# Kernel optimization log

Measured on AMD Instinct MI355X. Metric: run time of the kernel, lower is better.

## Reference

```python
import jax, jax.numpy as jnp
import numpy as np
from jax import lax

B, C, IMG = 16, 3, 256
NH, NRH, K, D = 128, 32, 512, 64
COMMITMENT = 0.25
DN = ('NCHW', 'OIHW', 'NCHW')


def _conv(x, w, b=None, stride=1, pad=1):
    out = lax.conv_general_dilated(x, w, (stride, stride), [(pad, pad), (pad, pad)], dimension_numbers=DN)
    if b is not None:
        out = out + b[None, :, None, None]
    return out


def _res(x, wa, wb):
    # Residual: x + ReLU(Conv1x1(ReLU(Conv3x3(x)))), convs bias-free
    h = jax.nn.relu(_conv(x, wa, None, 1, 1))
    h = jax.nn.relu(_conv(h, wb, None, 1, 0))
    return x + h


def _convT(x, w, b):
    # PyTorch ConvTranspose2d(k=4, s=2, p=1); w is torch layout (Cin, Cout, 4, 4)
    k = jnp.flip(w, (2, 3)).transpose(1, 0, 2, 3)  # -> OIHW
    out = lax.conv_general_dilated(x, k, (1, 1), [(2, 2), (2, 2)], lhs_dilation=(2, 2), dimension_numbers=DN)
    return out + b[None, :, None, None]


def setup_inputs():
    ks = iter(jax.random.split(jax.random.key(0), 32))
    def rn(shape, s=0.02):
        return jax.random.normal(next(ks), shape, jnp.float32) * s
    return dict(
        x=jax.random.normal(next(ks), (B, C, IMG, IMG), jnp.float32),
        emb=jax.random.uniform(next(ks), (K, D), jnp.float32, -1.0 / K, 1.0 / K),
        ew1=rn((NH // 2, C, 4, 4)), eb1=jnp.zeros((NH // 2,), jnp.float32),
        ew2=rn((NH, NH // 2, 4, 4)), eb2=jnp.zeros((NH,), jnp.float32),
        er1a=rn((NRH, NH, 3, 3)), er1b=rn((NH, NRH, 1, 1)),
        er2a=rn((NRH, NH, 3, 3)), er2b=rn((NH, NRH, 1, 1)),
        ew3=rn((D, NH, 3, 3)), eb3=jnp.zeros((D,), jnp.float32),
        dw1=rn((NH, D, 3, 3)), db1=jnp.zeros((NH,), jnp.float32),
        dr1a=rn((NRH, NH, 3, 3)), dr1b=rn((NH, NRH, 1, 1)),
        dr2a=rn((NRH, NH, 3, 3)), dr2b=rn((NH, NRH, 1, 1)),
        dtw1=rn((NH, NH // 2, 4, 4)), dtb1=jnp.zeros((NH // 2,), jnp.float32),
        dtw2=rn((NH // 2, C, 4, 4)), dtb2=jnp.zeros((C,), jnp.float32),
    )


def reference(x, emb, ew1, eb1, ew2, eb2, er1a, er1b, er2a, er2b, ew3, eb3,
              dw1, db1, dr1a, dr1b, dr2a, dr2b, dtw1, dtb1, dtw2, dtb2):
    # ---- encoder ----
    h = jax.nn.relu(_conv(x, ew1, eb1, 2, 1))
    h = jax.nn.relu(_conv(h, ew2, eb2, 2, 1))
    h = _res(h, er1a, er1b)
    h = _res(h, er2a, er2b)
    z = _conv(h, ew3, eb3, 1, 1)  # [B, D, H', W']

    # ---- vector quantization ----
    inputs = z.transpose(0, 2, 3, 1)              # BHWC
    flat = inputs.reshape(-1, emb.shape[1])        # [N, D]
    dist = (jnp.sum(flat ** 2, axis=1, keepdims=True)
            + jnp.sum(emb ** 2, axis=1)
            - 2.0 * flat @ emb.T)                  # [N, K]
    idx = jnp.argmin(dist, axis=1)                 # [N]
    quantized = emb[idx].reshape(inputs.shape)     # gather == one-hot matmul

    e_latent_loss = jnp.mean((lax.stop_gradient(quantized) - inputs) ** 2)
    q_latent_loss = jnp.mean((quantized - lax.stop_gradient(inputs)) ** 2)
    vq_loss = q_latent_loss + COMMITMENT * e_latent_loss

    quantized = inputs + lax.stop_gradient(quantized - inputs)  # straight-through
    q = quantized.transpose(0, 3, 1, 2)            # back to NCHW

    # ---- decoder ----
    h = _conv(q, dw1, db1, 1, 1)
    h = _res(h, dr1a, dr1b)
    h = _res(h, dr2a, dr2b)
    h = jax.nn.relu(_convT(h, dtw1, dtb1))
    out = jax.nn.relu(_convT(h, dtw2, dtb2))
    return out, vq_loss
```

## Files before the change

### kernel.cpp

```cpp
#include <hip/hip_runtime.h>

static __device__ __forceinline__ float frelu(float v) { return v > 0.f ? v : 0.f; }

__global__ __launch_bounds__(256) void k_ew1(const float* __restrict__ x,
    const float* __restrict__ w, const float* __restrict__ bias, float* __restrict__ out)
{
    const int t = threadIdx.x;
    const int tile = blockIdx.x;
    const int bcg = blockIdx.y;
    const int b = bcg >> 3, cg = bcg & 7;
    const int oy0 = (tile >> 3) << 4, ox0 = (tile & 7) << 4;
    const int tx = t & 15, ty = t >> 4;
    const int iy0 = 2 * oy0 - 1, ix0 = 2 * ox0 - 1;

    __shared__ float s_in[3 * 34 * 35];
    for (int i = t; i < 3 * 1156; i += 256) {
        int ci = i / 1156, r = (i % 1156) / 34, c = i % 34;
        int gy = iy0 + r, gx = ix0 + c;
        float v = 0.f;
        if ((unsigned)gy < 256u && (unsigned)gx < 256u)
            v = x[((b * 3 + ci) * 256 + gy) * 256 + gx];
        s_in[(ci * 34 + r) * 35 + c] = v;
    }
    __syncthreads();

    float acc[8];
#pragma unroll
    for (int i = 0; i < 8; ++i) acc[i] = 0.f;
#pragma unroll
    for (int ci = 0; ci < 3; ++ci)
#pragma unroll
        for (int ky = 0; ky < 4; ++ky)
#pragma unroll
            for (int kx = 0; kx < 4; ++kx) {
                float v = s_in[(ci * 34 + 2 * ty + ky) * 35 + 2 * tx + kx];
#pragma unroll
                for (int co = 0; co < 8; ++co)
                    acc[co] += v * w[((cg * 8 + co) * 3 + ci) * 16 + ky * 4 + kx];
            }
#pragma unroll
    for (int co = 0; co < 8; ++co) {
        int oc = cg * 8 + co;
        out[((b * 64 + oc) * 128 + oy0 + ty) * 128 + ox0 + tx] = frelu(acc[co] + bias[oc]);
    }
}

__global__ __launch_bounds__(256) void k_ew2(const float* __restrict__ in,
    const float* __restrict__ w, const float* __restrict__ bias, float* __restrict__ out)
{
    const int t = threadIdx.x;
    const int tile = blockIdx.x;
    const int bcg = blockIdx.y;
    const int b = bcg >> 4, cg = bcg & 15;
    const int oy0 = (tile >> 2) << 4, ox0 = (tile & 3) << 4;
    const int tx = t & 15, ty = t >> 4;
    const int iy0 = 2 * oy0 - 1, ix0 = 2 * ox0 - 1;

    __shared__ float s_in[4 * 34 * 35];
    float acc[8];
#pragma unroll
    for (int i = 0; i < 8; ++i) acc[i] = 0.f;

    for (int cc = 0; cc < 16; ++cc) {
        __syncthreads();
        for (int i = t; i < 4 * 1156; i += 256) {
            int ci = i / 1156, r = (i % 1156) / 34, c = i % 34;
            int gy = iy0 + r, gx = ix0 + c;
            float v = 0.f;
            if ((unsigned)gy < 128u && (unsigned)gx < 128u)
                v = in[((b * 64 + cc * 4 + ci) * 128 + gy) * 128 + gx];
            s_in[(ci * 34 + r) * 35 + c] = v;
        }
        __syncthreads();
#pragma unroll
        for (int ci = 0; ci < 4; ++ci)
#pragma unroll
            for (int ky = 0; ky < 4; ++ky)
#pragma unroll
                for (int kx = 0; kx < 4; ++kx) {
                    float v = s_in[(ci * 34 + 2 * ty + ky) * 35 + 2 * tx + kx];
#pragma unroll
                    for (int co = 0; co < 8; ++co)
                        acc[co] += v * w[((cg * 8 + co) * 64 + cc * 4 + ci) * 16 + ky * 4 + kx];
                }
    }
#pragma unroll
    for (int co = 0; co < 8; ++co) {
        int oc = cg * 8 + co;
        out[((b * 128 + oc) * 64 + oy0 + ty) * 64 + ox0 + tx] = frelu(acc[co] + bias[oc]);
    }
}

template<int CIN, int COUT, bool RELU, bool HASBIAS>
__global__ __launch_bounds__(256) void k_conv3(const float* __restrict__ in,
    const float* __restrict__ w, const float* __restrict__ bias, float* __restrict__ out)
{
    const int t = threadIdx.x;
    const int tile = blockIdx.x;
    const int bcg = blockIdx.y;
    const int b = bcg / (COUT / 8), cg = bcg % (COUT / 8);
    const int oy0 = (tile >> 2) << 4, ox0 = (tile & 3) << 4;
    const int tx = t & 15, ty = t >> 4;
    const int iy0 = oy0 - 1, ix0 = ox0 - 1;

    __shared__ float s_in[8 * 18 * 19];
    float acc[8];
#pragma unroll
    for (int i = 0; i < 8; ++i) acc[i] = 0.f;

    for (int cc = 0; cc < CIN / 8; ++cc) {
        __syncthreads();
        for (int i = t; i < 8 * 324; i += 256) {
            int ci = i / 324, r = (i % 324) / 18, c = i % 18;
            int gy = iy0 + r, gx = ix0 + c;
            float v = 0.f;
            if ((unsigned)gy < 64u && (unsigned)gx < 64u)
                v = in[((b * CIN + cc * 8 + ci) * 64 + gy) * 64 + gx];
            s_in[(ci * 18 + r) * 19 + c] = v;
        }
        __syncthreads();
#pragma unroll
        for (int ci = 0; ci < 8; ++ci)
#pragma unroll
            for (int ky = 0; ky < 3; ++ky)
#pragma unroll
                for (int kx = 0; kx < 3; ++kx) {
                    float v = s_in[(ci * 18 + ty + ky) * 19 + tx + kx];
#pragma unroll
                    for (int co = 0; co < 8; ++co)
                        acc[co] += v * w[((cg * 8 + co) * CIN + cc * 8 + ci) * 9 + ky * 3 + kx];
                }
    }
#pragma unroll
    for (int co = 0; co < 8; ++co) {
        int oc = cg * 8 + co;
        float v = acc[co];
        if (HASBIAS) v += bias[oc];
        if (RELU) v = frelu(v);
        out[((b * COUT + oc) * 64 + oy0 + ty) * 64 + ox0 + tx] = v;
    }
}

__global__ __launch_bounds__(256) void k_res1x1(const float* __restrict__ tin,
    const float* __restrict__ w, float* __restrict__ xbuf)
{
    int gid = blockIdx.x * 256 + threadIdx.x;
    int px = gid & 4095;
    int cg = (gid >> 12) & 7;
    int b = gid >> 15;
    float acc[16];
#pragma unroll
    for (int i = 0; i < 16; ++i) acc[i] = 0.f;
#pragma unroll
    for (int ci = 0; ci < 32; ++ci) {
        float v = tin[(b * 32 + ci) * 4096 + px];
#pragma unroll
        for (int co = 0; co < 16; ++co)
            acc[co] += v * w[(cg * 16 + co) * 32 + ci];
    }
#pragma unroll
    for (int co = 0; co < 16; ++co) {
        int o = (b * 128 + cg * 16 + co) * 4096 + px;
        xbuf[o] = xbuf[o] + frelu(acc[co]);
    }
}

__global__ __launch_bounds__(256) void k_vq(const float* __restrict__ z,
    const float* __restrict__ emb, int* __restrict__ idx, float* __restrict__ part)
{
    const int t = threadIdx.x;
    const int p = blockIdx.x * 256 + t;
    const int b = p >> 12, h = (p >> 6) & 63, wq = p & 63;
    float zr[64];
#pragma unroll
    for (int d = 0; d < 64; ++d)
        zr[d] = z[((b * 64 + d) * 64 + h) * 64 + wq];

    __shared__ float se[64 * 64];
    float best = 3.4e38f;
    int bi = 0;
    for (int ch = 0; ch < 8; ++ch) {
        __syncthreads();
#pragma unroll
        for (int i = 0; i < 16; ++i)
            se[i * 256 + t] = emb[ch * 4096 + i * 256 + t];
        __syncthreads();
        for (int e = 0; e < 64; ++e) {
            float dist = 0.f;
#pragma unroll
            for (int d = 0; d < 64; ++d) {
                float diff = zr[d] - se[e * 64 + d];
                dist += diff * diff;
            }
            if (dist < best) { best = dist; bi = ch * 64 + e; }
        }
    }
    idx[p] = bi;

    float s = best;
#pragma unroll
    for (int off = 32; off > 0; off >>= 1) s += __shfl_down(s, off, 64);
    __shared__ float sw[4];
    if ((t & 63) == 0) sw[t >> 6] = s;
    __syncthreads();
    if (t == 0) part[blockIdx.x] = sw[0] + sw[1] + sw[2] + sw[3];
}

__global__ __launch_bounds__(256) void k_qbuild(const int* __restrict__ idx,
    const float* __restrict__ emb, float* __restrict__ q)
{
    int i = blockIdx.x * 256 + threadIdx.x;
    int wq = i & 63;
    int h = (i >> 6) & 63;
    int d = (i >> 12) & 63;
    int b = i >> 18;
    int p = (b << 12) | (h << 6) | wq;
    q[i] = emb[idx[p] * 64 + d];
}

__global__ __launch_bounds__(256) void k_loss(const float* __restrict__ part, float* __restrict__ out)
{
    int t = threadIdx.x;
    float s = part[t];
#pragma unroll
    for (int off = 32; off > 0; off >>= 1) s += __shfl_down(s, off, 64);
    __shared__ float sw[4];
    if ((t & 63) == 0) sw[t >> 6] = s;
    __syncthreads();
    if (t == 0) out[3145728] = 1.25f * (sw[0] + sw[1] + sw[2] + sw[3]) / 4194304.0f;
}

template<int CIN, int COUT, int COT, int OW>
__global__ __launch_bounds__(256) void k_convT(const float* __restrict__ in,
    const float* __restrict__ w, const float* __restrict__ bias, float* __restrict__ out)
{
    const int IW = OW / 2;
    const int TPR = OW / 32;
    const int t = threadIdx.x;
    const int tile = blockIdx.x;
    const int NCG = COUT / COT;
    const int bcg = blockIdx.y;
    const int b = bcg / NCG, cg = bcg % NCG;
    const int oy0 = (tile / TPR) * 32, ox0 = (tile % TPR) * 32;
    const int tx = t & 15, ty = t >> 4;
    const int iy0 = oy0 / 2 - 1, ix0 = ox0 / 2 - 1;

    __shared__ float s_in[8 * 18 * 19];
    float acc[4][COT];
#pragma unroll
    for (int a = 0; a < 4; ++a)
#pragma unroll
        for (int c = 0; c < COT; ++c) acc[a][c] = 0.f;

    for (int cc = 0; cc < CIN / 8; ++cc) {
        __syncthreads();
        for (int i = t; i < 8 * 324; i += 256) {
            int ci = i / 324, r = (i % 324) / 18, c = i % 18;
            int gy = iy0 + r, gx = ix0 + c;
            float v = 0.f;
            if ((unsigned)gy < (unsigned)IW && (unsigned)gx < (unsigned)IW)
                v = in[((b * CIN + cc * 8 + ci) * IW + gy) * IW + gx];
            s_in[(ci * 18 + r) * 19 + c] = v;
        }
        __syncthreads();
#pragma unroll
        for (int ci = 0; ci < 8; ++ci) {
            float rr[3][3];
#pragma unroll
            for (int dy = 0; dy < 3; ++dy)
#pragma unroll
                for (int dx = 0; dx < 3; ++dx)
                    rr[dy][dx] = s_in[(ci * 18 + ty + dy) * 19 + tx + dx];
#pragma unroll
            for (int ky = 0; ky < 4; ++ky) {
                const int py = 1 - (ky & 1);
                const int dy = (ky == 0) ? 2 : (ky == 3) ? 0 : 1;
#pragma unroll
                for (int kx = 0; kx < 4; ++kx) {
                    const int pxr = 1 - (kx & 1);
                    const int dx = (kx == 0) ? 2 : (kx == 3) ? 0 : 1;
                    float v = rr[dy][dx];
#pragma unroll
                    for (int co = 0; co < COT; ++co)
                        acc[py * 2 + pxr][co] +=
                            v * w[((cc * 8 + ci) * COUT + cg * COT + co) * 16 + ky * 4 + kx];
                }
            }
        }
    }
    const int ye = oy0 + 2 * ty, xe = ox0 + 2 * tx;
#pragma unroll
    for (int py = 0; py < 2; ++py)
#pragma unroll
        for (int pxr = 0; pxr < 2; ++pxr)
#pragma unroll
            for (int co = 0; co < COT; ++co) {
                int oc = cg * COT + co;
                out[((b * COUT + oc) * OW + ye + py) * OW + xe + pxr] =
                    frelu(acc[py * 2 + pxr][co] + bias[oc]);
            }
}

extern "C" void kernel_launch(void* const* d_in, const int* in_sizes, int n_in,
                              void* d_out, int out_size, void* d_ws, size_t ws_size,
                              hipStream_t stream)
{
    (void)in_sizes; (void)n_in; (void)out_size; (void)ws_size;
    const float* x    = (const float*)d_in[0];
    const float* emb  = (const float*)d_in[1];
    const float* ew1  = (const float*)d_in[2];
    const float* eb1  = (const float*)d_in[3];
    const float* ew2  = (const float*)d_in[4];
    const float* eb2  = (const float*)d_in[5];
    const float* er1a = (const float*)d_in[6];
    const float* er1b = (const float*)d_in[7];
    const float* er2a = (const float*)d_in[8];
    const float* er2b = (const float*)d_in[9];
    const float* ew3w = (const float*)d_in[10];
    const float* eb3  = (const float*)d_in[11];
    const float* dw1  = (const float*)d_in[12];
    const float* db1  = (const float*)d_in[13];
    const float* dr1a = (const float*)d_in[14];
    const float* dr1b = (const float*)d_in[15];
    const float* dr2a = (const float*)d_in[16];
    const float* dr2b = (const float*)d_in[17];
    const float* dtw1 = (const float*)d_in[18];
    const float* dtb1 = (const float*)d_in[19];
    const float* dtw2 = (const float*)d_in[20];
    const float* dtb2 = (const float*)d_in[21];
    float* out = (float*)d_out;
    float* ws  = (float*)d_ws;

    float* A   = ws;
    float* Bf  = ws + 16777216;
    float* T   = ws;
    float* Z   = ws + 2097152;
    float* Q   = ws + 6291456;
    int*   IDX = (int*)(ws + 10485760);
    float* PART= ws + 10551296;

    k_ew1<<<dim3(64, 128), 256, 0, stream>>>(x, ew1, eb1, A);
    k_ew2<<<dim3(16, 256), 256, 0, stream>>>(A, ew2, eb2, Bf);
    k_conv3<128, 32, true, false><<<dim3(16, 64), 256, 0, stream>>>(Bf, er1a, nullptr, T);
    k_res1x1<<<2048, 256, 0, stream>>>(T, er1b, Bf);
    k_conv3<128, 32, true, false><<<dim3(16, 64), 256, 0, stream>>>(Bf, er2a, nullptr, T);
    k_res1x1<<<2048, 256, 0, stream>>>(T, er2b, Bf);
    k_conv3<128, 64, false, true><<<dim3(16, 128), 256, 0, stream>>>(Bf, ew3w, eb3, Z);
    k_vq<<<256, 256, 0, stream>>>(Z, emb, IDX, PART);
    k_qbuild<<<16384, 256, 0, stream>>>(IDX, emb, Q);
    k_loss<<<1, 256, 0, stream>>>(PART, out);
    k_conv3<64, 128, false, true><<<dim3(16, 256), 256, 0, stream>>>(Q, dw1, db1, Bf);
    k_conv3<128, 32, true, false><<<dim3(16, 64), 256, 0, stream>>>(Bf, dr1a, nullptr, T);
    k_res1x1<<<2048, 256, 0, stream>>>(T, dr1b, Bf);
    k_conv3<128, 32, true, false><<<dim3(16, 64), 256, 0, stream>>>(Bf, dr2a, nullptr, T);
    k_res1x1<<<2048, 256, 0, stream>>>(T, dr2b, Bf);
    k_convT<128, 64, 8, 128><<<dim3(16, 128), 256, 0, stream>>>(Bf, dtw1, dtb1, A);
    k_convT<64, 3, 3, 256><<<dim3(64, 16), 256, 0, stream>>>(A, dtw2, dtb2, out);
}
```

Measured before the change: 2.810 ms.

## Widen output-channel tiles, prefetch inputs into registers, split VQ search and tile q-build

Several kernels now compute more output channels per thread: ew1 does all 64, ew2 and several conv3 and convT launches do 16. This cuts redundant input tile loads and block count. Each conv kernel now prefetches the next channel chunk into registers while computing the current one, and ew2 stores its input tile in a parity-split (polyphase) layout. The VQ search is split across four codebook slices plus a reduce kernel to raise parallelism, and q-build transposes through shared memory for coalesced writes. The trade-off is more registers per thread, which can lower occupancy.

Measured after the change: 8.076 ms. 2.87x slower.

```diff
diff --git a/kernel.cpp b/kernel.cpp
--- a/kernel.cpp
+++ b/kernel.cpp
@@ -7,15 +7,14 @@
 {
     const int t = threadIdx.x;
     const int tile = blockIdx.x;
-    const int bcg = blockIdx.y;
-    const int b = bcg >> 3, cg = bcg & 7;
+    const int b = blockIdx.y;
     const int oy0 = (tile >> 3) << 4, ox0 = (tile & 7) << 4;
     const int tx = t & 15, ty = t >> 4;
     const int iy0 = 2 * oy0 - 1, ix0 = 2 * ox0 - 1;
 
     __shared__ float s_in[3 * 34 * 35];
     for (int i = t; i < 3 * 1156; i += 256) {
-        int ci = i / 1156, r = (i % 1156) / 34, c = i % 34;
+        int ci = i / 1156, rem = i % 1156, r = rem / 34, c = rem % 34;
         int gy = iy0 + r, gx = ix0 + c;
         float v = 0.f;
         if ((unsigned)gy < 256u && (unsigned)gx < 256u)
@@ -24,25 +23,26 @@
     }
     __syncthreads();
 
-    float acc[8];
-#pragma unroll
-    for (int i = 0; i < 8; ++i) acc[i] = 0.f;
-#pragma unroll
-    for (int ci = 0; ci < 3; ++ci)
+    float acc[64];
+#pragma unroll
+    for (int i = 0; i < 64; ++i) acc[i] = 0.f;
+#pragma unroll
+    for (int ci = 0; ci < 3; ++ci) {
+        float v[16];
 #pragma unroll
         for (int ky = 0; ky < 4; ++ky)
 #pragma unroll
-            for (int kx = 0; kx < 4; ++kx) {
-                float v = s_in[(ci * 34 + 2 * ty + ky) * 35 + 2 * tx + kx];
-#pragma unroll
-                for (int co = 0; co < 8; ++co)
-                    acc[co] += v * w[((cg * 8 + co) * 3 + ci) * 16 + ky * 4 + kx];
-            }
-#pragma unroll
-    for (int co = 0; co < 8; ++co) {
-        int oc = cg * 8 + co;
-        out[((b * 64 + oc) * 128 + oy0 + ty) * 128 + ox0 + tx] = frelu(acc[co] + bias[oc]);
-    }
+            for (int kx = 0; kx < 4; ++kx)
+                v[ky * 4 + kx] = s_in[(ci * 34 + 2 * ty + ky) * 35 + 2 * tx + kx];
+#pragma unroll
+        for (int co = 0; co < 64; ++co)
+#pragma unroll
+            for (int k = 0; k < 16; ++k)
+                acc[co] += v[k] * w[(co * 3 + ci) * 16 + k];
+    }
+#pragma unroll
+    for (int co = 0; co < 64; ++co)
+        out[((b * 64 + co) * 128 + oy0 + ty) * 128 + ox0 + tx] = frelu(acc[co] + bias[co]);
 }
 
 __global__ __launch_bounds__(256) void k_ew2(const float* __restrict__ in,
@@ -51,93 +51,149 @@
     const int t = threadIdx.x;
     const int tile = blockIdx.x;
     const int bcg = blockIdx.y;
-    const int b = bcg >> 4, cg = bcg & 15;
+    const int b = bcg >> 3, cg = bcg & 7;
     const int oy0 = (tile >> 2) << 4, ox0 = (tile & 3) << 4;
     const int tx = t & 15, ty = t >> 4;
     const int iy0 = 2 * oy0 - 1, ix0 = 2 * ox0 - 1;
 
-    __shared__ float s_in[4 * 34 * 35];
-    float acc[8];
-#pragma unroll
-    for (int i = 0; i < 8; ++i) acc[i] = 0.f;
-
+    __shared__ float s_in[4 * 4 * 17 * 18];
+
+    constexpr int NS = 19;
+    int goff[NS], loff[NS];
+#pragma unroll
+    for (int k = 0; k < NS; ++k) {
+        int idx = t + (k << 8);
+        if (idx < 4624) {
+            int ci = idx / 1156, rem = idx % 1156, r = rem / 34, c = rem % 34;
+            loff[k] = ((ci * 4 + (r & 1) * 2 + (c & 1)) * 17 + (r >> 1)) * 18 + (c >> 1);
+            int gy = iy0 + r, gx = ix0 + c;
+            goff[k] = ((unsigned)gy < 128u && (unsigned)gx < 128u)
+                      ? ((b * 64 + ci) * 128 + gy) * 128 + gx : -1;
+        } else { loff[k] = -1; goff[k] = -1; }
+    }
+
+    float acc[16];
+#pragma unroll
+    for (int i = 0; i < 16; ++i) acc[i] = 0.f;
+    float pre[NS];
+#pragma unroll
+    for (int k = 0; k < NS; ++k) pre[k] = (goff[k] >= 0) ? in[goff[k]] : 0.f;
+#pragma unroll
+    for (int k = 0; k < NS; ++k) if (loff[k] >= 0) s_in[loff[k]] = pre[k];
+    __syncthreads();
+
+#pragma unroll 1
     for (int cc = 0; cc < 16; ++cc) {
+        if (cc < 15) {
+            const int coff = (cc + 1) * 4 * 16384;
+#pragma unroll
+            for (int k = 0; k < NS; ++k)
+                pre[k] = (goff[k] >= 0) ? in[goff[k] + coff] : 0.f;
+        }
+#pragma unroll
+        for (int ci = 0; ci < 4; ++ci) {
+            float v[16];
+#pragma unroll
+            for (int ky = 0; ky < 4; ++ky)
+#pragma unroll
+                for (int kx = 0; kx < 4; ++kx)
+                    v[ky * 4 + kx] = s_in[((ci * 4 + (ky & 1) * 2 + (kx & 1)) * 17
+                                           + ty + (ky >> 1)) * 18 + tx + (kx >> 1)];
+#pragma unroll
+            for (int co = 0; co < 16; ++co)
+#pragma unroll
+                for (int k = 0; k < 16; ++k)
+                    acc[co] += v[k] * w[((cg * 16 + co) * 64 + cc * 4 + ci) * 16 + k];
+        }
         __syncthreads();
-        for (int i = t; i < 4 * 1156; i += 256) {
-            int ci = i / 1156, r = (i % 1156) / 34, c = i % 34;
-            int gy = iy0 + r, gx = ix0 + c;
-            float v = 0.f;
-            if ((unsigned)gy < 128u && (unsigned)gx < 128u)
-                v = in[((b * 64 + cc * 4 + ci) * 128 + gy) * 128 + gx];
-            s_in[(ci * 34 + r) * 35 + c] = v;
-        }
-        __syncthreads();
-#pragma unroll
-        for (int ci = 0; ci < 4; ++ci)
-#pragma unroll
-            for (int ky = 0; ky < 4; ++ky)
-#pragma unroll
-                for (int kx = 0; kx < 4; ++kx) {
-                    float v = s_in[(ci * 34 + 2 * ty + ky) * 35 + 2 * tx + kx];
-#pragma unroll
-                    for (int co = 0; co < 8; ++co)
-                        acc[co] += v * w[((cg * 8 + co) * 64 + cc * 4 + ci) * 16 + ky * 4 + kx];
-                }
-    }
-#pragma unroll
-    for (int co = 0; co < 8; ++co) {
-        int oc = cg * 8 + co;
+        if (cc < 15) {
+#pragma unroll
+            for (int k = 0; k < NS; ++k) if (loff[k] >= 0) s_in[loff[k]] = pre[k];
+            __syncthreads();
+        }
+    }
+#pragma unroll
+    for (int co = 0; co < 16; ++co) {
+        int oc = cg * 16 + co;
         out[((b * 128 + oc) * 64 + oy0 + ty) * 64 + ox0 + tx] = frelu(acc[co] + bias[oc]);
     }
 }
 
-template<int CIN, int COUT, bool RELU, bool HASBIAS>
+template<int CIN, int COUT, int COT, bool RELU, bool HASBIAS>
 __global__ __launch_bounds__(256) void k_conv3(const float* __restrict__ in,
     const float* __restrict__ w, const float* __restrict__ bias, float* __restrict__ out)
 {
     const int t = threadIdx.x;
     const int tile = blockIdx.x;
+    constexpr int NCG = COUT / COT;
     const int bcg = blockIdx.y;
-    const int b = bcg / (COUT / 8), cg = bcg % (COUT / 8);
+    const int b = bcg / NCG, cg = bcg % NCG;
     const int oy0 = (tile >> 2) << 4, ox0 = (tile & 3) << 4;
     const int tx = t & 15, ty = t >> 4;
     const int iy0 = oy0 - 1, ix0 = ox0 - 1;
+    constexpr int NC = CIN / 8;
 
     __shared__ float s_in[8 * 18 * 19];
-    float acc[8];
-#pragma unroll
-    for (int i = 0; i < 8; ++i) acc[i] = 0.f;
-
-    for (int cc = 0; cc < CIN / 8; ++cc) {
+    constexpr int NS = 11;
+    int goff[NS], loff[NS];
+#pragma unroll
+    for (int k = 0; k < NS; ++k) {
+        int idx = t + (k << 8);
+        if (idx < 2592) {
+            int ci = idx / 324, rem = idx % 324, r = rem / 18, c = rem % 18;
+            loff[k] = (ci * 18 + r) * 19 + c;
+            int gy = iy0 + r, gx = ix0 + c;
+            goff[k] = ((unsigned)gy < 64u && (unsigned)gx < 64u)
+                      ? ((b * CIN + ci) * 64 + gy) * 64 + gx : -1;
+        } else { loff[k] = -1; goff[k] = -1; }
+    }
+
+    float acc[COT];
+#pragma unroll
+    for (int i = 0; i < COT; ++i) acc[i] = 0.f;
+    float pre[NS];
+#pragma unroll
+    for (int k = 0; k < NS; ++k) pre[k] = (goff[k] >= 0) ? in[goff[k]] : 0.f;
+#pragma unroll
+    for (int k = 0; k < NS; ++k) if (loff[k] >= 0) s_in[loff[k]] = pre[k];
+    __syncthreads();
+
+#pragma unroll 1
+    for (int cc = 0; cc < NC; ++cc) {
+        if (cc < NC - 1) {
+            const int coff = (cc + 1) * 8 * 4096;
+#pragma unroll
+            for (int k = 0; k < NS; ++k)
+                pre[k] = (goff[k] >= 0) ? in[goff[k] + coff] : 0.f;
+        }
+#pragma unroll
+        for (int ci = 0; ci < 8; ++ci) {
+            float v[9];
+#pragma unroll
+            for (int ky = 0; ky < 3; ++ky)
+#pragma unroll
+                for (int kx = 0; kx < 3; ++kx)
+                    v[ky * 3 + kx] = s_in[(ci * 18 + ty + ky) * 19 + tx + kx];
+#pragma unroll
+            for (int co = 0; co < COT; ++co)
+#pragma unroll
+                for (int k = 0; k < 9; ++k)
+                    acc[co] += v[k] * w[((cg * COT + co) * CIN + cc * 8 + ci) * 9 + k];
+        }
         __syncthreads();
-        for (int i = t; i < 8 * 324; i += 256) {
-            int ci = i / 324, r = (i % 324) / 18, c = i % 18;
-            int gy = iy0 + r, gx = ix0 + c;
-            float v = 0.f;
-            if ((unsigned)gy < 64u && (unsigned)gx < 64u)
-                v = in[((b * CIN + cc * 8 + ci) * 64 + gy) * 64 + gx];
-            s_in[(ci * 18 + r) * 19 + c] = v;
-        }
-        __syncthreads();
-#pragma unroll
-        for (int ci = 0; ci < 8; ++ci)
-#pragma unroll
-            for (int ky = 0; ky < 3; ++ky)
-#pragma unroll
-                for (int kx = 0; kx < 3; ++kx) {
-                    float v = s_in[(ci * 18 + ty + ky) * 19 + tx + kx];
-#pragma unroll
-                    for (int co = 0; co < 8; ++co)
-                        acc[co] += v * w[((cg * 8 + co) * CIN + cc * 8 + ci) * 9 + ky * 3 + kx];
-                }
-    }
-#pragma unroll
-    for (int co = 0; co < 8; ++co) {
-        int oc = cg * 8 + co;
-        float v = acc[co];
-        if (HASBIAS) v += bias[oc];
-        if (RELU) v = frelu(v);
-        out[((b * COUT + oc) * 64 + oy0 + ty) * 64 + ox0 + tx] = v;
+        if (cc < NC - 1) {
+#pragma unroll
+            for (int k = 0; k < NS; ++k) if (loff[k] >= 0) s_in[loff[k]] = pre[k];
+            __syncthreads();
+        }
+    }
+#pragma unroll
+    for (int co = 0; co < COT; ++co) {
+        int oc = cg * COT + co;
+        float vv = acc[co];
+        if (HASBIAS) vv += bias[oc];
+        if (RELU) vv = frelu(vv);
+        out[((b * COUT + oc) * 64 + oy0 + ty) * 64 + ox0 + tx] = vv;
     }
 }
 
@@ -165,38 +221,47 @@
     }
 }
 
-__global__ __launch_bounds__(256) void k_vq(const float* __restrict__ z,
-    const float* __restrict__ emb, int* __restrict__ idx, float* __restrict__ part)
-{
-    const int t = threadIdx.x;
-    const int p = blockIdx.x * 256 + t;
-    const int b = p >> 12, h = (p >> 6) & 63, wq = p & 63;
+__global__ __launch_bounds__(256) void k_vq1(const float* __restrict__ z,
+    const float* __restrict__ emb, float* __restrict__ distb, int* __restrict__ idxb)
+{
+    const int gid = blockIdx.x * 256 + threadIdx.x;
+    const int px = gid & 65535, slice = gid >> 16;
+    const int b = px >> 12, h = (px >> 6) & 63, wq = px & 63;
     float zr[64];
 #pragma unroll
     for (int d = 0; d < 64; ++d)
         zr[d] = z[((b * 64 + d) * 64 + h) * 64 + wq];
 
-    __shared__ float se[64 * 64];
-    float best = 3.4e38f;
-    int bi = 0;
-    for (int ch = 0; ch < 8; ++ch) {
-        __syncthreads();
-#pragma unroll
-        for (int i = 0; i < 16; ++i)
-            se[i * 256 + t] = emb[ch * 4096 + i * 256 + t];
-        __syncthreads();
-        for (int e = 0; e < 64; ++e) {
-            float dist = 0.f;
-#pragma unroll
-            for (int d = 0; d < 64; ++d) {
-                float diff = zr[d] - se[e * 64 + d];
-                dist += diff * diff;
-            }
-            if (dist < best) { best = dist; bi = ch * 64 + e; }
-        }
-    }
-    idx[p] = bi;
-
+    float best = 3.4e38f; int bi = 0;
+    const int e0 = slice * 128;
+#pragma unroll 1
+    for (int e = 0; e < 128; ++e) {
+        const float* er = emb + (e0 + e) * 64;
+        float dist = 0.f;
+#pragma unroll
+        for (int d = 0; d < 64; ++d) {
+            float df = zr[d] - er[d];
+            dist += df * df;
+        }
+        if (dist < best) { best = dist; bi = e0 + e; }
+    }
+    distb[gid] = best;
+    idxb[gid] = bi;
+}
+
+__global__ __launch_bounds__(256) void k_vq2(const float* __restrict__ distb,
+    const int* __restrict__ idxb, int* __restrict__ idx, float* __restrict__ part)
+{
+    const int t = threadIdx.x;
+    const int px = blockIdx.x * 256 + t;
+    float best = distb[px]; int bi = idxb[px];
+#pragma unroll
+    for (int s2 = 1; s2 < 4; ++s2) {
+        float d = distb[s2 * 65536 + px];
+        int i2 = idxb[s2 * 65536 + px];
+        if (d < best) { best = d; bi = i2; }
+    }
+    idx[px] = bi;
     float s = best;
 #pragma unroll
     for (int off = 32; off > 0; off >>= 1) s += __shfl_down(s, off, 64);
@@ -209,16 +274,30 @@
 __global__ __launch_bounds__(256) void k_qbuild(const int* __restrict__ idx,
     const float* __restrict__ emb, float* __restrict__ q)
 {
-    int i = blockIdx.x * 256 + threadIdx.x;
-    int wq = i & 63;
-    int h = (i >> 6) & 63;
-    int d = (i >> 12) & 63;
-    int b = i >> 18;
-    int p = (b << 12) | (h << 6) | wq;
-    q[i] = emb[idx[p] * 64 + d];
-}
-
-__global__ __launch_bounds__(256) void k_loss(const float* __restrict__ part, float* __restrict__ out)
+    const int t = threadIdx.x;
+    const int bh = blockIdx.x;
+    const int b = bh >> 6, h = bh & 63;
+    __shared__ int s_idx[64];
+    __shared__ float s_e[64 * 65];
+    if (t < 64) s_idx[t] = idx[(b << 12) | (h << 6) | t];
+    __syncthreads();
+#pragma unroll
+    for (int k = 0; k < 16; ++k) {
+        int i = t + (k << 8);
+        int wq = i >> 6, d = i & 63;
+        s_e[wq * 65 + d] = emb[s_idx[wq] * 64 + d];
+    }
+    __syncthreads();
+#pragma unroll
+    for (int k = 0; k < 16; ++k) {
+        int i = t + (k << 8);
+        int d = i >> 6, wq = i & 63;
+        q[((b * 64 + d) * 64 + h) * 64 + wq] = s_e[wq * 65 + d];
+    }
+}
+
+__global__ __launch_bounds__(256) void k_loss(const float* __restrict__ part,
+    float* __restrict__ out)
 {
     int t = threadIdx.x;
     float s = part[t];
@@ -234,35 +313,53 @@
 __global__ __launch_bounds__(256) void k_convT(const float* __restrict__ in,
     const float* __restrict__ w, const float* __restrict__ bias, float* __restrict__ out)
 {
-    const int IW = OW / 2;
-    const int TPR = OW / 32;
+    constexpr int IW = OW / 2;
+    constexpr int TPR = OW / 32;
     const int t = threadIdx.x;
     const int tile = blockIdx.x;
-    const int NCG = COUT / COT;
+    constexpr int NCG = COUT / COT;
     const int bcg = blockIdx.y;
     const int b = bcg / NCG, cg = bcg % NCG;
     const int oy0 = (tile / TPR) * 32, ox0 = (tile % TPR) * 32;
     const int tx = t & 15, ty = t >> 4;
     const int iy0 = oy0 / 2 - 1, ix0 = ox0 / 2 - 1;
+    constexpr int NC = CIN / 8;
 
     __shared__ float s_in[8 * 18 * 19];
+    constexpr int NS = 11;
+    int goff[NS], loff[NS];
+#pragma unroll
+    for (int k = 0; k < NS; ++k) {
+        int idx = t + (k << 8);
+        if (idx < 2592) {
+            int ci = idx / 324, rem = idx % 324, r = rem / 18, c = rem % 18;
+            loff[k] = (ci * 18 + r) * 19 + c;
+            int gy = iy0 + r, gx = ix0 + c;
+            goff[k] = ((unsigned)gy < (unsigned)IW && (unsigned)gx < (unsigned)IW)
+                      ? ((b * CIN + ci) * IW + gy) * IW + gx : -1;
+        } else { loff[k] = -1; goff[k] = -1; }
+    }
+
     float acc[4][COT];
 #pragma unroll
     for (int a = 0; a < 4; ++a)
 #pragma unroll
         for (int c = 0; c < COT; ++c) acc[a][c] = 0.f;
-
-    for (int cc = 0; cc < CIN / 8; ++cc) {
-        __syncthreads();
-        for (int i = t; i < 8 * 324; i += 256) {
-            int ci = i / 324, r = (i % 324) / 18, c = i % 18;
-            int gy = iy0 + r, gx = ix0 + c;
-            float v = 0.f;
-            if ((unsigned)gy < (unsigned)IW && (unsigned)gx < (unsigned)IW)
-                v = in[((b * CIN + cc * 8 + ci) * IW + gy) * IW + gx];
-            s_in[(ci * 18 + r) * 19 + c] = v;
-        }
-        __syncthreads();
+    float pre[NS];
+#pragma unroll
+    for (int k = 0; k < NS; ++k) pre[k] = (goff[k] >= 0) ? in[goff[k]] : 0.f;
+#pragma unroll
+    for (int k = 0; k < NS; ++k) if (loff[k] >= 0) s_in[loff[k]] = pre[k];
+    __syncthreads();
+
+#pragma unroll 1
+    for (int cc = 0; cc < NC; ++cc) {
+        if (cc < NC - 1) {
+            const int coff = (cc + 1) * 8 * IW * IW;
+#pragma unroll
+            for (int k = 0; k < NS; ++k)
+                pre[k] = (goff[k] >= 0) ? in[goff[k] + coff] : 0.f;
+        }
 #pragma unroll
         for (int ci = 0; ci < 8; ++ci) {
             float rr[3][3];
@@ -272,20 +369,25 @@
                 for (int dx = 0; dx < 3; ++dx)
                     rr[dy][dx] = s_in[(ci * 18 + ty + dy) * 19 + tx + dx];
 #pragma unroll
-            for (int ky = 0; ky < 4; ++ky) {
-                const int py = 1 - (ky & 1);
-                const int dy = (ky == 0) ? 2 : (ky == 3) ? 0 : 1;
-#pragma unroll
-                for (int kx = 0; kx < 4; ++kx) {
-                    const int pxr = 1 - (kx & 1);
-                    const int dx = (kx == 0) ? 2 : (kx == 3) ? 0 : 1;
-                    float v = rr[dy][dx];
-#pragma unroll
-                    for (int co = 0; co < COT; ++co)
-                        acc[py * 2 + pxr][co] +=
-                            v * w[((cc * 8 + ci) * COUT + cg * COT + co) * 16 + ky * 4 + kx];
+            for (int co = 0; co < COT; ++co)
+#pragma unroll
+                for (int ky = 0; ky < 4; ++ky) {
+                    const int py = 1 - (ky & 1);
+                    const int dy = (ky == 0) ? 2 : (ky == 3) ? 0 : 1;
+#pragma unroll
+                    for (int kx = 0; kx < 4; ++kx) {
+                        const int pxr = 1 - (kx & 1);
+                        const int dx = (kx == 0) ? 2 : (kx == 3) ? 0 : 1;
+                        acc[py * 2 + pxr][co] += rr[dy][dx]
+                            * w[((cc * 8 + ci) * COUT + cg * COT + co) * 16 + ky * 4 + kx];
+                    }
                 }
-            }
+        }
+        __syncthreads();
+        if (cc < NC - 1) {
+#pragma unroll
+            for (int k = 0; k < NS; ++k) if (loff[k] >= 0) s_in[loff[k]] = pre[k];
+            __syncthreads();
         }
     }
     const int ye = oy0 + 2 * ty, xe = ox0 + 2 * tx;
@@ -331,29 +433,32 @@
     float* out = (float*)d_out;
     float* ws  = (float*)d_ws;
 
-    float* A   = ws;
-    float* Bf  = ws + 16777216;
-    float* T   = ws;
-    float* Z   = ws + 2097152;
-    float* Q   = ws + 6291456;
-    int*   IDX = (int*)(ws + 10485760);
-    float* PART= ws + 10551296;
-
-    k_ew1<<<dim3(64, 128), 256, 0, stream>>>(x, ew1, eb1, A);
-    k_ew2<<<dim3(16, 256), 256, 0, stream>>>(A, ew2, eb2, Bf);
-    k_conv3<128, 32, true, false><<<dim3(16, 64), 256, 0, stream>>>(Bf, er1a, nullptr, T);
+    float* A    = ws;
+    float* Bf   = ws + 16777216;
+    float* T    = ws;
+    float* Z    = ws + 2097152;
+    float* Q    = ws + 6291456;
+    int*   IDX  = (int*)(ws + 10485760);
+    float* PART = ws + 10551296;
+    float* DISTB= ws + 10552064;
+    int*   IDXB = (int*)(ws + 10814208);
+
+    k_ew1<<<dim3(64, 16), 256, 0, stream>>>(x, ew1, eb1, A);
+    k_ew2<<<dim3(16, 128), 256, 0, stream>>>(A, ew2, eb2, Bf);
+    k_conv3<128, 32, 8, true, false><<<dim3(16, 64), 256, 0, stream>>>(Bf, er1a, nullptr, T);
     k_res1x1<<<2048, 256, 0, stream>>>(T, er1b, Bf);
-    k_conv3<128, 32, true, false><<<dim3(16, 64), 256, 0, stream>>>(Bf, er2a, nullptr, T);
+    k_conv3<128, 32, 8, true, false><<<dim3(16, 64), 256, 0, stream>>>(Bf, er2a, nullptr, T);
     k_res1x1<<<2048, 256, 0, stream>>>(T, er2b, Bf);
-    k_conv3<128, 64, false, true><<<dim3(16, 128), 256, 0, stream>>>(Bf, ew3w, eb3, Z);
-    k_vq<<<256, 256, 0, stream>>>(Z, emb, IDX, PART);
-    k_qbuild<<<16384, 256, 0, stream>>>(IDX, emb, Q);
+    k_conv3<128, 64, 16, false, true><<<dim3(16, 64), 256, 0, stream>>>(Bf, ew3w, eb3, Z);
+    k_vq1<<<1024, 256, 0, stream>>>(Z, emb, DISTB, IDXB);
+    k_vq2<<<256, 256, 0, stream>>>(DISTB, IDXB, IDX, PART);
     k_loss<<<1, 256, 0, stream>>>(PART, out);
-    k_conv3<64, 128, false, true><<<dim3(16, 256), 256, 0, stream>>>(Q, dw1, db1, Bf);
-    k_conv3<128, 32, true, false><<<dim3(16, 64), 256, 0, stream>>>(Bf, dr1a, nullptr, T);
+    k_qbuild<<<1024, 256, 0, stream>>>(IDX, emb, Q);
+    k_conv3<64, 128, 16, false, true><<<dim3(16, 128), 256, 0, stream>>>(Q, dw1, db1, Bf);
+    k_conv3<128, 32, 8, true, false><<<dim3(16, 64), 256, 0, stream>>>(Bf, dr1a, nullptr, T);
     k_res1x1<<<2048, 256, 0, stream>>>(T, dr1b, Bf);
-    k_conv3<128, 32, true, false><<<dim3(16, 64), 256, 0, stream>>>(Bf, dr2a, nullptr, T);
+    k_conv3<128, 32, 8, true, false><<<dim3(16, 64), 256, 0, stream>>>(Bf, dr2a, nullptr, T);
     k_res1x1<<<2048, 256, 0, stream>>>(T, dr2b, Bf);
-    k_convT<128, 64, 8, 128><<<dim3(16, 128), 256, 0, stream>>>(Bf, dtw1, dtb1, A);
+    k_convT<128, 64, 16, 128><<<dim3(16, 64), 256, 0, stream>>>(Bf, dtw1, dtb1, A);
     k_convT<64, 3, 3, 256><<<dim3(64, 16), 256, 0, stream>>>(A, dtw2, dtb2, out);
 }
```
